# Optimization experiments

Measured on AMD Instinct MI355X. Metric: run time of the kernel, lower is better.

## Reference

```python
import jax, jax.numpy as jnp
import numpy as np

N_ATOMS = 131072
N_EDGES = 524288
N_MOLS = 2048
D = 128      # n_atom_basis
F = 128      # n_filters
G = 50       # n_gaussians
T = 3        # interaction blocks
CUTOFF = 5.0
LOG2 = float(np.log(2.0))


def ssp(x):
    # shifted softplus: ln(0.5*e^x + 0.5) = softplus(x) - ln 2
    return jax.nn.softplus(x) - LOG2


def setup_inputs() -> dict:
    key = jax.random.key(0)
    ks = jax.random.split(key, 20)
    s = 0.05
    z = jax.random.randint(ks[0], (N_ATOMS,), 1, 100, dtype=jnp.int32)
    xyz = jax.random.normal(ks[1], (N_ATOMS, 3), dtype=jnp.float32) * 3.0
    a0 = jax.random.randint(ks[2], (N_EDGES,), 0, N_ATOMS, dtype=jnp.int32)
    off = jax.random.randint(ks[3], (N_EDGES,), 1, N_ATOMS, dtype=jnp.int32)
    a = jnp.stack([a0, (a0 + off) % N_ATOMS], axis=1)  # distinct endpoints
    mol_id = jnp.sort(jax.random.randint(ks[4], (N_ATOMS,), 0, N_MOLS, dtype=jnp.int32))
    emb = (jax.random.normal(ks[5], (100, D)) * s).at[0].set(0.0)  # padding_idx=0
    return dict(
        xyz=xyz,
        emb=emb,
        fw1=jax.random.normal(ks[6], (T, G, F)) * s,
        fb1=jnp.zeros((T, F)),
        fw2=jax.random.normal(ks[7], (T, F, F)) * s,
        fb2=jnp.zeros((T, F)),
        win=jax.random.normal(ks[8], (T, D, F)) * s,
        wout1=jax.random.normal(ks[9], (T, F, D)) * s,
        bout1=jnp.zeros((T, D)),
        wout2=jax.random.normal(ks[10], (T, D, D)) * s,
        bout2=jnp.zeros((T, D)),
        wa1=jax.random.normal(ks[11], (D, D // 2)) * s,
        ba1=jnp.zeros((D // 2,)),
        wa2=jax.random.normal(ks[12], (D // 2, 1)) * s,
        ba2=jnp.zeros((1,)),
        z=z, a=a, mol_id=mol_id,
    )


def reference(xyz, emb, fw1, fb1, fw2, fb2, win, wout1, bout1, wout2, bout2,
              wa1, ba1, wa2, ba2, z, a, mol_id):
    r = emb[z]                                            # [N, D] atom embeddings
    # edge distances: e = ||xyz[a0] - xyz[a1]||  -> [E, 1]
    d = jnp.sqrt(((xyz[a[:, 0]] - xyz[a[:, 1]]) ** 2).sum(-1))[:, None]
    # Gaussian smearing on [0, cutoff]
    offsets = jnp.linspace(0.0, CUTOFF, G)
    width = offsets[1] - offsets[0]
    g = jnp.exp((-0.5 / width ** 2) * (d - offsets) ** 2)  # [E, G]
    # smooth cosine cutoff (cutoff_soft)
    C = 0.5 * (jnp.cos(d * jnp.pi / CUTOFF) + 1.0)          # [E, 1]
    for t in range(T):
        # continuous filter network on edge features
        W = ssp(g @ fw1[t] + fb1[t]) @ fw2[t] + fb2[t]      # [E, F]
        W = W * C
        h = r @ win[t]                                      # in2f, no bias [N, F]
        # symmetric gather-filter-scatter over undirected edge list
        y = jnp.zeros_like(h)
        y = y.at[a[:, 0]].add(h[a[:, 1]] * W)
        y = y.at[a[:, 1]].add(h[a[:, 0]] * W)
        dr = ssp(y @ wout1[t] + bout1[t]) @ wout2[t] + bout2[t]
        r = r + dr                                          # residual update
    # atomwise energy head
    r = ssp(r @ wa1 + ba1) @ wa2 + ba2                      # [N, 1]
    # per-molecule sum pooling (torch.split + sum)
    return jax.ops.segment_sum(r, mol_id, num_segments=N_MOLS)  # [N_MOLS, 1]
```

## Files before the change

kernel.cpp:

```cpp
#include <hip/hip_runtime.h>
#include <hip/hip_bf16.h>

#define N_ATOMS 131072
#define N_EDGES 524288
#define N_MOLS  2048
#define DD      128
#define FF      128
#define GG      50
#define TT      3

typedef __hip_bfloat16 bf16;
typedef __attribute__((ext_vector_type(8))) short short8;
typedef __attribute__((ext_vector_type(4))) float floatx4;

__device__ __forceinline__ float b2f(bf16 v) { return __bfloat162float(v); }
__device__ __forceinline__ bf16  f2b(float v) { return __float2bfloat16(v); }

__device__ __forceinline__ unsigned short f2bu(float f) {
    unsigned u = __float_as_uint(f);
    u += 0x7fff + ((u >> 16) & 1);
    return (unsigned short)(u >> 16);
}
__device__ __forceinline__ bf16 f2b_fast(float f) {
    union { unsigned short u; bf16 b; } c; c.u = f2bu(f); return c.b;
}
__device__ __forceinline__ unsigned int pk2(float lo, float hi) {
    return ((unsigned)f2bu(hi) << 16) | f2bu(lo);
}

__device__ __forceinline__ float2 up2(unsigned int u) {
    float2 f;
    f.x = __uint_as_float(u << 16);
    f.y = __uint_as_float(u & 0xffff0000u);
    return f;
}

__device__ __forceinline__ float sspf(float x) {
    float e = __expf(-fabsf(x));
    return fmaxf(x, 0.f) + __logf(1.f + e) - 0.69314718056f;
}

__device__ __forceinline__ void fma8(float* ac, uint4 wv, uint4 hv) {
    float2 w0 = up2(wv.x), h0 = up2(hv.x);
    float2 w1 = up2(wv.y), h1 = up2(hv.y);
    float2 w2 = up2(wv.z), h2 = up2(hv.z);
    float2 w3 = up2(wv.w), h3 = up2(hv.w);
    ac[0] = fmaf(w0.x, h0.x, ac[0]); ac[1] = fmaf(w0.y, h0.y, ac[1]);
    ac[2] = fmaf(w1.x, h1.x, ac[2]); ac[3] = fmaf(w1.y, h1.y, ac[3]);
    ac[4] = fmaf(w2.x, h2.x, ac[4]); ac[5] = fmaf(w2.y, h2.y, ac[5]);
    ac[6] = fmaf(w3.x, h3.x, ac[6]); ac[7] = fmaf(w3.y, h3.y, ac[7]);
}

template <int NCT>
__device__ __forceinline__ void mfma_half(const bf16* A, const bf16* B,
                                          floatx4 (&acc)[2][NCT],
                                          int kA, int wave, int q, int ln) {
#pragma unroll
    for (int k0 = 0; k0 < 64; k0 += 32) {
        short8 a0 = *(const short8*)(A + (wave * 32 + ln) * 136 + kA + k0 + q * 8);
        short8 a1 = *(const short8*)(A + (wave * 32 + 16 + ln) * 136 + kA + k0 + q * 8);
#pragma unroll
        for (int ct = 0; ct < NCT; ct++) {
            short8 b = *(const short8*)(B + (ct * 16 + ln) * 72 + k0 + q * 8);
            acc[0][ct] = __builtin_amdgcn_mfma_f32_16x16x32_bf16(a0, b, acc[0][ct], 0, 0, 0);
            acc[1][ct] = __builtin_amdgcn_mfma_f32_16x16x32_bf16(a1, b, acc[1][ct], 0, 0, 0);
        }
    }
}

template <int NCT>
__device__ __forceinline__ void mfma64(const bf16* A, const bf16* B,
                                       floatx4 (&acc)[NCT],
                                       int kA, int wave, int q, int ln) {
#pragma unroll
    for (int k0 = 0; k0 < 64; k0 += 32) {
        short8 a = *(const short8*)(A + (wave * 16 + ln) * 136 + kA + k0 + q * 8);
#pragma unroll
        for (int ct = 0; ct < NCT; ct++) {
            short8 b = *(const short8*)(B + (ct * 16 + ln) * 72 + k0 + q * 8);
            acc[ct] = __builtin_amdgcn_mfma_f32_16x16x32_bf16(a, b, acc[ct], 0, 0, 0);
        }
    }
}

__device__ __forceinline__ void stage_b(bf16* B, const bf16* WT, int k0,
                                        int nrows, int ldk, int tid) {
    for (int i = tid; i < nrows * 8; i += 256) {
        int n = i >> 3, kc = i & 7;
        *(short8*)(B + n * 72 + kc * 8) =
            *(const short8*)(WT + n * ldk + k0 + kc * 8);
    }
}

__global__ __launch_bounds__(256) void k_init(const float* __restrict__ emb,
                                              const int* __restrict__ z,
                                              bf16* __restrict__ rb) {
    int idx = blockIdx.x * 256 + threadIdx.x;
    int atom = idx >> 4, seg = idx & 15;
    const float* src = emb + (size_t)z[atom] * DD + seg * 8;
    float4 v0 = *(const float4*)(src);
    float4 v1 = *(const float4*)(src + 4);
    uint4 o;
    o.x = pk2(v0.x, v0.y); o.y = pk2(v0.z, v0.w);
    o.z = pk2(v1.x, v1.y); o.w = pk2(v1.z, v1.w);
    *(uint4*)(rb + (size_t)atom * DD + seg * 8) = o;
}

__global__ __launch_bounds__(256) void k_dist(const float* __restrict__ xyz,
                                              const int* __restrict__ a,
                                              float* __restrict__ dArr,
                                              float* __restrict__ cArr,
                                              float* __restrict__ molE) {
    int e = blockIdx.x * 256 + threadIdx.x;
    if (e < N_MOLS) molE[e] = 0.f;
    int A0 = a[2 * e], A1 = a[2 * e + 1];
    float dx = xyz[3 * A0]     - xyz[3 * A1];
    float dy = xyz[3 * A0 + 1] - xyz[3 * A1 + 1];
    float dz = xyz[3 * A0 + 2] - xyz[3 * A1 + 2];
    float d = sqrtf(dx * dx + dy * dy + dz * dz);
    dArr[e] = d;
    cArr[e] = 0.5f * (__cosf(d * 0.6283185307179586f) + 1.f);
}

__global__ __launch_bounds__(256) void k_wt(const float* __restrict__ fw1,
                                            const float* __restrict__ fw2,
                                            const float* __restrict__ win,
                                            const float* __restrict__ wout1,
                                            const float* __restrict__ wout2,
                                            const float* __restrict__ wa1,
                                            bf16* __restrict__ fw1T, bf16* __restrict__ fw2T,
                                            bf16* __restrict__ winT, bf16* __restrict__ wout1T,
                                            bf16* __restrict__ wout2T, bf16* __restrict__ wa1T) {
    int idx = blockIdx.x * 256 + threadIdx.x;
    if (idx < 3 * 128 * 64) {
        int t = idx / 8192, j = idx % 8192;
        int n = j >> 6, k = j & 63;
        fw1T[idx] = (k < GG) ? f2b(fw1[t * GG * FF + k * FF + n]) : f2b(0.f);
        return;
    }
    idx -= 3 * 128 * 64;
    if (idx < 3 * 16384) { int t = idx / 16384, j = idx % 16384; int n = j >> 7, k = j & 127;
        fw2T[idx] = f2b(fw2[t * 16384 + k * 128 + n]); return; }
    idx -= 3 * 16384;
    if (idx < 3 * 16384) { int t = idx / 16384, j = idx % 16384; int n = j >> 7, k = j & 127;
        winT[idx] = f2b(win[t * 16384 + k * 128 + n]); return; }
    idx -= 3 * 16384;
    if (idx < 3 * 16384) { int t = idx / 16384, j = idx % 16384; int n = j >> 7, k = j & 127;
        wout1T[idx] = f2b(wout1[t * 16384 + k * 128 + n]); return; }
    idx -= 3 * 16384;
    if (idx < 3 * 16384) { int t = idx / 16384, j = idx % 16384; int n = j >> 7, k = j & 127;
        wout2T[idx] = f2b(wout2[t * 16384 + k * 128 + n]); return; }
    idx -= 3 * 16384;
    if (idx < 64 * 128) { int n = idx >> 7, k = idx & 127;
        wa1T[idx] = f2b(wa1[k * 64 + n]); return; }
}

__global__ __launch_bounds__(256) void k_zero(int* __restrict__ p, int n) {
    int i = blockIdx.x * 256 + threadIdx.x;
    if (i < n) p[i] = 0;
}

__global__ __launch_bounds__(256) void k_count2(const int* __restrict__ a,
                                                int* __restrict__ cntA,
                                                int* __restrict__ cnt1,
                                                float* __restrict__ molE) {
    int e = blockIdx.x * 256 + threadIdx.x;
    if (e < N_MOLS) molE[e] = 0.f;
    atomicAdd(&cntA[a[2 * e]], 1);
    atomicAdd(&cnt1[a[2 * e + 1]], 1);
}

__global__ __launch_bounds__(256) void k_scan1(const int* __restrict__ counts,
                                               int* __restrict__ bsum) {
    __shared__ int red[256];
    int tid = threadIdx.x;
    int i0 = blockIdx.x * 512 + tid * 2;
    red[tid] = counts[i0] + counts[i0 + 1];
    __syncthreads();
    for (int off = 128; off > 0; off >>= 1) {
        if (tid < off) red[tid] += red[tid + off];
        __syncthreads();
    }
    if (tid == 0) bsum[blockIdx.x] = red[0];
}

__global__ __launch_bounds__(256) void k_scan2(int* __restrict__ bsum,
                                               int* __restrict__ ptr) {
    __shared__ int v[256];
    int tid = threadIdx.x;
    v[tid] = bsum[tid];
    __syncthreads();
    if (tid == 0) {
        int acc = 0;
        for (int i = 0; i < 256; i++) { int t = v[i]; v[i] = acc; acc += t; }
        ptr[N_ATOMS] = acc;
    }
    __syncthreads();
    bsum[tid] = v[tid];
}

__global__ __launch_bounds__(256) void k_scan3(int* __restrict__ counts,
                                               const int* __restrict__ bsum,
                                               int* __restrict__ ptr) {
    __shared__ int red[256];
    int tid = threadIdx.x;
    int i0 = blockIdx.x * 512 + tid * 2;
    int c0 = counts[i0], c1 = counts[i0 + 1];
    int s = c0 + c1;
    red[tid] = s;
    __syncthreads();
    for (int off = 1; off < 256; off <<= 1) {
        int t = (tid >= off) ? red[tid - off] : 0;
        __syncthreads();
        red[tid] += t;
        __syncthreads();
    }
    int base = bsum[blockIdx.x] + red[tid] - s;
    ptr[i0] = base;
    ptr[i0 + 1] = base + c0;
    counts[i0] = base;
    counts[i0 + 1] = base + c0;
}

__global__ __launch_bounds__(256) void k_permA(const float* __restrict__ xyz,
                                               const int* __restrict__ a,
                                               int* __restrict__ cursorA,
                                               int* __restrict__ cursor1,
                                               float* __restrict__ dAp,
                                               float* __restrict__ cAp,
                                               int* __restrict__ a1s,
                                               int* __restrict__ adj1) {
    int e = blockIdx.x * 256 + threadIdx.x;
    int A0 = a[2 * e], A1 = a[2 * e + 1];
    float dx = xyz[3 * A0]     - xyz[3 * A1];
    float dy = xyz[3 * A0 + 1] - xyz[3 * A1 + 1];
    float dz = xyz[3 * A0 + 2] - xyz[3 * A1 + 2];
    float d = sqrtf(dx * dx + dy * dy + dz * dz);
    int newe = atomicAdd(&cursorA[A0], 1);
    dAp[newe] = d;
    cAp[newe] = 0.5f * (__cosf(d * 0.6283185307179586f) + 1.f);
    a1s[newe] = A1;
    int slot = atomicAdd(&cursor1[A1], 1);
    adj1[2 * slot] = newe;
    adj1[2 * slot + 1] = A0;
}

struct SmemHE {
    bf16 A[64][136];
    bf16 B[128][72];
    float dS[64], cS[64], b1S[128], b2S[128];
};

__device__ __forceinline__ void h_part(SmemHE& sm, int blk,
                                       const bf16* __restrict__ rb,
                                       const bf16* __restrict__ winT_t,
                                       bf16* __restrict__ h) {
    int tid = threadIdx.x, n0 = blk * 64;
    for (int i = tid; i < 64 * 16; i += 256) {
        int row = i >> 4, seg = i & 15;
        *(uint4*)(&sm.A[row][seg * 8]) =
            *(const uint4*)(rb + (size_t)(n0 + row) * DD + seg * 8);
    }
    stage_b(&sm.B[0][0], winT_t, 0, 128, 128, tid);
    __syncthreads();
    int wave = tid >> 6, lane = tid & 63, q = lane >> 4, ln = lane & 15;
    floatx4 acc[8];
#pragma unroll
    for (int j = 0; j < 8; j++) acc[j] = (floatx4){0.f, 0.f, 0.f, 0.f};
    mfma64<8>(&sm.A[0][0], &sm.B[0][0], acc, 0, wave, q, ln);
    __syncthreads();
    stage_b(&sm.B[0][0], winT_t, 64, 128, 128, tid);
    __syncthreads();
    mfma64<8>(&sm.A[0][0], &sm.B[0][0], acc, 64, wave, q, ln);
#pragma unroll
    for (int ct = 0; ct < 8; ct++)
#pragma unroll
        for (int rg = 0; rg < 4; rg++) {
            int row = wave * 16 + q * 4 + rg, col = ct * 16 + ln;
            sm.A[row][col] = f2b_fast(acc[ct][rg]);
        }
    __syncthreads();
    for (int i = tid; i < 64 * 16; i += 256) {
        int row = i >> 4, seg = i & 15;
        *(uint4*)(h + (size_t)(n0 + row) * FF + seg * 8) =
            *(const uint4*)(&sm.A[row][seg * 8]);
    }
}

__device__ __forceinline__ void edge_part(SmemHE& sm, int blk,
                                          const float* __restrict__ dAp,
                                          const float* __restrict__ cAp,
                                          const bf16* __restrict__ fw1T_t,
                                          const float* __restrict__ fb1_t,
                                          const bf16* __restrict__ fw2T_t,
                                          const float* __restrict__ fb2_t,
                                          bf16* __restrict__ Wt) {
    int tid = threadIdx.x, e0 = blk * 64;
    if (tid < 64) { sm.dS[tid] = dAp[e0 + tid]; sm.cS[tid] = cAp[e0 + tid]; }
    if (tid < 128) { sm.b1S[tid] = fb1_t[tid]; sm.b2S[tid] = fb2_t[tid]; }
    stage_b(&sm.B[0][0], fw1T_t, 0, 128, 64, tid);
    __syncthreads();
    const float width = 5.0f / 49.0f;
    const float coeff = -0.5f / (width * width);
    for (int idx = tid; idx < 64 * 32; idx += 256) {
        int i = idx >> 5, kp = (idx & 31) * 2;
        float d = sm.dS[i];
        float t0 = d - (float)kp * width;
        float t1 = d - (float)(kp + 1) * width;
        float v0 = (kp < GG)     ? __expf(coeff * t0 * t0) : 0.f;
        float v1 = (kp + 1 < GG) ? __expf(coeff * t1 * t1) : 0.f;
        *(unsigned int*)(&sm.A[i][kp]) = pk2(v0, v1);
    }
    __syncthreads();
    int wave = tid >> 6, lane = tid & 63, q = lane >> 4, ln = lane & 15;
    floatx4 acc[8];
#pragma unroll
    for (int j = 0; j < 8; j++) acc[j] = (floatx4){0.f, 0.f, 0.f, 0.f};
    mfma64<8>(&sm.A[0][0], &sm.B[0][0], acc, 0, wave, q, ln);
#pragma unroll
    for (int ct = 0; ct < 8; ct++)
#pragma unroll
        for (int rg = 0; rg < 4; rg++) {
            int row = wave * 16 + q * 4 + rg, col = ct * 16 + ln;
            sm.A[row][col] = f2b_fast(sspf(acc[ct][rg] + sm.b1S[col]));
        }
    __syncthreads();
    stage_b(&sm.B[0][0], fw2T_t, 0, 128, 128, tid);
    __syncthreads();
#pragma unroll
    for (int j = 0; j < 8; j++) acc[j] = (floatx4){0.f, 0.f, 0.f, 0.f};
    mfma64<8>(&sm.A[0][0], &sm.B[0][0], acc, 0, wave, q, ln);
    __syncthreads();
    stage_b(&sm.B[0][0], fw2T_t, 64, 128, 128, tid);
    __syncthreads();
    mfma64<8>(&sm.A[0][0], &sm.B[0][0], acc, 64, wave, q, ln);
#pragma unroll
    for (int ct = 0; ct < 8; ct++)
#pragma unroll
        for (int rg = 0; rg < 4; rg++) {
            int row = wave * 16 + q * 4 + rg, col = ct * 16 + ln;
            sm.A[row][col] = f2b_fast((acc[ct][rg] + sm.b2S[col]) * sm.cS[row]);
        }
    __syncthreads();
    for (int i = tid; i < 64 * 16; i += 256) {
        int row = i >> 4, seg = i & 15;
        *(uint4*)(Wt + (size_t)(e0 + row) * FF + seg * 8) =
            *(const uint4*)(&sm.A[row][seg * 8]);
    }
}

__global__ __launch_bounds__(256, 4) void k_he(const bf16* __restrict__ rb,
                                               const bf16* __restrict__ winT_t,
                                               bf16* __restrict__ h,
                                               const float* __restrict__ dAp,
                                               const float* __restrict__ cAp,
                                               const bf16* __restrict__ fw1T_t,
                                               const float* __restrict__ fb1_t,
                                               const bf16* __restrict__ fw2T_t,
                                               const float* __restrict__ fb2_t,
                                               bf16* __restrict__ Wt) {
    __shared__ SmemHE sm;
    int bi = blockIdx.x;
    if (bi % 5 == 0)
        h_part(sm, bi / 5, rb, winT_t, h);
    else
        edge_part(sm, bi - bi / 5 - 1, dAp, cAp, fw1T_t, fb1_t, fw2T_t, fb2_t, Wt);
}

__global__ __launch_bounds__(256, 5) void k_gather_node64(const int* __restrict__ baseA,
                                                          const int* __restrict__ a1s,
                                                          const int* __restrict__ ptr1,
                                                          const int* __restrict__ adj1,
                                                          const bf16* __restrict__ Wt,
                                                          const bf16* __restrict__ h,
                                                          const bf16* __restrict__ wout1T_t,
                                                          const float* __restrict__ bo1_t,
                                                          const bf16* __restrict__ wout2T_t,
                                                          const float* __restrict__ bo2_t,
                                                          bf16* __restrict__ rb) {
    __shared__ __align__(16) bf16 A[64][136];
    __shared__ __align__(16) bf16 B[64][72];
    __shared__ float b1S[128], b2S[128];
    int tid = threadIdx.x, n0 = blockIdx.x * 64;
    if (tid < 128) { b1S[tid] = bo1_t[tid]; b2S[tid] = bo2_t[tid]; }
    stage_b(&B[0][0], wout1T_t, 0, 64, 128, tid);
    int wave = tid >> 6, lane = tid & 63;
    int seg = lane & 15;
    int rg  = lane >> 4;
    for (int k = 0; k < 16; k += 2) {
        int rowA = wave * 16 + k;
        int atomA = n0 + rowA;
        int2 b01 = *(const int2*)(baseA + atomA);
        int b2v = baseA[atomA + 2];
        int2 p01 = *(const int2*)(ptr1 + atomA);
        int p2v = ptr1[atomA + 2];
        int sA0 = b01.x + rg, eA0v = b01.y;
        int sB0 = b01.y + rg, eB0v = b2v;
        int sA1 = p01.x + rg, eA1v = p01.y;
        int sB1 = p01.y + rg, eB1v = p2v;
        int oA = (sA0 < eA0v) ? a1s[sA0] : 0;
        int oB = (sB0 < eB0v) ? a1s[sB0] : 0;
        int2 eoA = (sA1 < eA1v) ? *(const int2*)(adj1 + 2 * sA1) : make_int2(0, 0);
        int2 eoB = (sB1 < eB1v) ? *(const int2*)(adj1 + 2 * sB1) : make_int2(0, 0);
        float acA[8], acB[8];
#pragma unroll
        for (int j = 0; j < 8; j++) { acA[j] = 0.f; acB[j] = 0.f; }
        while ((sA0 < eA0v) | (sA1 < eA1v) | (sB0 < eB0v) | (sB1 < eB1v)) {
            bool pA0 = sA0 < eA0v, pA1 = sA1 < eA1v;
            bool pB0 = sB0 < eB0v, pB1 = sB1 < eB1v;
            uint4 wvA0, hvA0, wvA1, hvA1, wvB0, hvB0, wvB1, hvB1;
            if (pA0) {
                wvA0 = *(const uint4*)(Wt + (size_t)sA0 * FF + seg * 8);
                hvA0 = *(const uint4*)(h + (size_t)oA * FF + seg * 8);
            }
            if (pA1) {
                wvA1 = *(const uint4*)(Wt + (size_t)eoA.x * FF + seg * 8);
                hvA1 = *(const uint4*)(h + (size_t)eoA.y * FF + seg * 8);
            }
            if (pB0) {
                wvB0 = *(const uint4*)(Wt + (size_t)sB0 * FF + seg * 8);
                hvB0 = *(const uint4*)(h + (size_t)oB * FF + seg * 8);
            }
            if (pB1) {
                wvB1 = *(const uint4*)(Wt + (size_t)eoB.x * FF + seg * 8);
                hvB1 = *(const uint4*)(h + (size_t)eoB.y * FF + seg * 8);
            }
            int sA0n = sA0 + 4, sA1n = sA1 + 4, sB0n = sB0 + 4, sB1n = sB1 + 4;
            int oAn = (sA0n < eA0v) ? a1s[sA0n] : 0;
            int oBn = (sB0n < eB0v) ? a1s[sB0n] : 0;
            int2 eoAn = (sA1n < eA1v) ? *(const int2*)(adj1 + 2 * sA1n) : make_int2(0, 0);
            int2 eoBn = (sB1n < eB1v) ? *(const int2*)(adj1 + 2 * sB1n) : make_int2(0, 0);
            if (pA0) fma8(acA, wvA0, hvA0);
            if (pA1) fma8(acA, wvA1, hvA1);
            if (pB0) fma8(acB, wvB0, hvB0);
            if (pB1) fma8(acB, wvB1, hvB1);
            sA0 = sA0n; sA1 = sA1n; sB0 = sB0n; sB1 = sB1n;
            oA = oAn; oB = oBn; eoA = eoAn; eoB = eoBn;
        }
#pragma unroll
        for (int j = 0; j < 8; j++) {
            float vA = acA[j], vB = acB[j];
            vA += __shfl_down(vA, 32); vB += __shfl_down(vB, 32);
            vA += __shfl_down(vA, 16); vB += __shfl_down(vB, 16);
            acA[j] = vA; acB[j] = vB;
        }
        if (rg == 0) {
            uint4 oU;
            oU.x = pk2(acA[0], acA[1]); oU.y = pk2(acA[2], acA[3]);
            oU.z = pk2(acA[4], acA[5]); oU.w = pk2(acA[6], acA[7]);
            *(uint4*)(&A[rowA][seg * 8]) = oU;
            oU.x = pk2(acB[0], acB[1]); oU.y = pk2(acB[2], acB[3]);
            oU.z = pk2(acB[4], acB[5]); oU.w = pk2(acB[6], acB[7]);
            *(uint4*)(&A[rowA + 1][seg * 8]) = oU;
        }
    }
    __syncthreads();
    int q = lane >> 4, ln = lane & 15;
    floatx4 acc[8];
#pragma unroll
    for (int j = 0; j < 8; j++) acc[j] = (floatx4){0.f, 0.f, 0.f, 0.f};
    mfma64<4>(&A[0][0], &B[0][0], *(floatx4(*)[4])(&acc[0]), 0, wave, q, ln);
    __syncthreads();
    stage_b(&B[0][0], wout1T_t + 64 * 128, 0, 64, 128, tid);
    __syncthreads();
    mfma64<4>(&A[0][0], &B[0][0], *(floatx4(*)[4])(&acc[4]), 0, wave, q, ln);
    __syncthreads();
    stage_b(&B[0][0], wout1T_t, 64, 64, 128, tid);
    __syncthreads();
    mfma64<4>(&A[0][0], &B[0][0], *(floatx4(*)[4])(&acc[0]), 64, wave, q, ln);
    __syncthreads();
    stage_b(&B[0][0], wout1T_t + 64 * 128, 64, 64, 128, tid);
    __syncthreads();
    mfma64<4>(&A[0][0], &B[0][0], *(floatx4(*)[4])(&acc[4]), 64, wave, q, ln);
#pragma unroll
    for (int cc = 0; cc < 8; cc++)
#pragma unroll
        for (int rgi = 0; rgi < 4; rgi++) {
            int row = wave * 16 + q * 4 + rgi;
            int col = (cc >> 2) * 64 + (cc & 3) * 16 + ln;
            A[row][col] = f2b_fast(sspf(acc[cc][rgi] + b1S[col]));
        }
    __syncthreads();
    stage_b(&B[0][0], wout2T_t, 0, 64, 128, tid);
    __syncthreads();
#pragma unroll
    for (int j = 0; j < 8; j++) acc[j] = (floatx4){0.f, 0.f, 0.f, 0.f};
    mfma64<4>(&A[0][0], &B[0][0], *(floatx4(*)[4])(&acc[0]), 0, wave, q, ln);
    __syncthreads();
    stage_b(&B[0][0], wout2T_t + 64 * 128, 0, 64, 128, tid);
    __syncthreads();
    mfma64<4>(&A[0][0], &B[0][0], *(floatx4(*)[4])(&acc[4]), 0, wave, q, ln);
    __syncthreads();
    stage_b(&B[0][0], wout2T_t, 64, 64, 128, tid);
    __syncthreads();
    mfma64<4>(&A[0][0], &B[0][0], *(floatx4(*)[4])(&acc[0]), 64, wave, q, ln);
    __syncthreads();
    stage_b(&B[0][0], wout2T_t + 64 * 128, 64, 64, 128, tid);
    __syncthreads();
    mfma64<4>(&A[0][0], &B[0][0], *(floatx4(*)[4])(&acc[4]), 64, wave, q, ln);
#pragma unroll
    for (int cc = 0; cc < 8; cc++)
#pragma unroll
        for (int rgi = 0; rgi < 4; rgi++) {
            int row = wave * 16 + q * 4 + rgi;
            int col = (cc >> 2) * 64 + (cc & 3) * 16 + ln;
            size_t off = (size_t)(n0 + row) * DD + col;
            rb[off] = f2b_fast(b2f(rb[off]) + acc[cc][rgi] + b2S[col]);
        }
}

__global__ __launch_bounds__(256) void k_h(const bf16* __restrict__ rb,
                                           const bf16* __restrict__ winT_t,
                                           bf16* __restrict__ h,
                                           float* __restrict__ y) {
    __shared__ __align__(16) bf16 A[128][136];
    __shared__ __align__(16) bf16 B[128][72];
    int tid = threadIdx.x, n0 = blockIdx.x * 128;
    for (int i = tid; i < 128 * 16; i += 256) {
        int row = i >> 4, seg = i & 15;
        *(uint4*)(&A[row][seg * 8]) =
            *(const uint4*)(rb + (size_t)(n0 + row) * DD + seg * 8);
        *(float4*)(y + (size_t)(n0 + row) * FF + seg * 8) = (float4){0.f, 0.f, 0.f, 0.f};
        *(float4*)(y + (size_t)(n0 + row) * FF + seg * 8 + 4) = (float4){0.f, 0.f, 0.f, 0.f};
    }
    stage_b(&B[0][0], winT_t, 0, 128, 128, tid);
    __syncthreads();
    int wave = tid >> 6, lane = tid & 63, q = lane >> 4, ln = lane & 15;
    floatx4 acc[2][8];
#pragma unroll
    for (int i = 0; i < 2; i++)
#pragma unroll
        for (int j = 0; j < 8; j++) acc[i][j] = (floatx4){0.f, 0.f, 0.f, 0.f};
    mfma_half<8>(&A[0][0], &B[0][0], acc, 0, wave, q, ln);
    __syncthreads();
    stage_b(&B[0][0], winT_t, 64, 128, 128, tid);
    __syncthreads();
    mfma_half<8>(&A[0][0], &B[0][0], acc, 64, wave, q, ln);
#pragma unroll
    for (int rt = 0; rt < 2; rt++)
#pragma unroll
        for (int ct = 0; ct < 8; ct++)
#pragma unroll
            for (int rg = 0; rg < 4; rg++) {
                int row = wave * 32 + rt * 16 + q * 4 + rg, col = ct * 16 + ln;
                h[(size_t)(n0 + row) * FF + col] = f2b(acc[rt][ct][rg]);
            }
}

__global__ __launch_bounds__(256) void k_edge(const float* __restrict__ dArr,
                                              const float* __restrict__ cArr,
                                              const int* __restrict__ a,
                                              const bf16* __restrict__ fw1T_t,
                                              const float* __restrict__ fb1_t,
                                              const bf16* __restrict__ fw2T_t,
                                              const float* __restrict__ fb2_t,
                                              const bf16* __restrict__ h,
                                              float* __restrict__ y) {
    __shared__ __align__(16) bf16 A[128][136];
    __shared__ __align__(16) bf16 B[128][72];
    __shared__ float dS[128], cS[128], b1S[128], b2S[128];
    __shared__ int a0S[128], a1S[128];
    int tid = threadIdx.x, e0 = blockIdx.x * 128;
    if (tid < 128) {
        int e = e0 + tid;
        dS[tid] = dArr[e]; cS[tid] = cArr[e];
        a0S[tid] = a[2 * e]; a1S[tid] = a[2 * e + 1];
        b1S[tid] = fb1_t[tid]; b2S[tid] = fb2_t[tid];
    }
    stage_b(&B[0][0], fw1T_t, 0, 128, 64, tid);
    __syncthreads();
    const float width = 5.0f / 49.0f;
    const float coeff = -0.5f / (width * width);
    for (int idx = tid; idx < 128 * 64; idx += 256) {
        int i = idx >> 6, k = idx & 63;
        float v = 0.f;
        if (k < GG) { float t = dS[i] - (float)k * width; v = __expf(coeff * t * t); }
        A[i][k] = f2b(v);
// ... 55 lines not shown
    int tid = threadIdx.x, n0 = blockIdx.x * 128;
    if (tid < 128) { b1S[tid] = bo1_t[tid]; b2S[tid] = bo2_t[tid]; }
    for (int idx = tid; idx < 128 * 128; idx += 256) {
        int row = idx >> 7, col = idx & 127;
        A[row][col] = f2b(y[(size_t)(n0 + row) * FF + col]);
    }
    stage_b(&B[0][0], wout1T_t, 0, 128, 128, tid);
    __syncthreads();
    int wave = tid >> 6, lane = tid & 63, q = lane >> 4, ln = lane & 15;
    floatx4 acc[2][8];
#pragma unroll
    for (int i = 0; i < 2; i++)
#pragma unroll
        for (int j = 0; j < 8; j++) acc[i][j] = (floatx4){0.f, 0.f, 0.f, 0.f};
    mfma_half<8>(&A[0][0], &B[0][0], acc, 0, wave, q, ln);
    __syncthreads();
    stage_b(&B[0][0], wout1T_t, 64, 128, 128, tid);
    __syncthreads();
    mfma_half<8>(&A[0][0], &B[0][0], acc, 64, wave, q, ln);
#pragma unroll
    for (int rt = 0; rt < 2; rt++)
#pragma unroll
        for (int ct = 0; ct < 8; ct++)
#pragma unroll
            for (int rg = 0; rg < 4; rg++) {
                int row = wave * 32 + rt * 16 + q * 4 + rg, col = ct * 16 + ln;
                A[row][col] = f2b(sspf(acc[rt][ct][rg] + b1S[col]));
            }
    __syncthreads();
    stage_b(&B[0][0], wout2T_t, 0, 128, 128, tid);
    __syncthreads();
#pragma unroll
    for (int i = 0; i < 2; i++)
#pragma unroll
        for (int j = 0; j < 8; j++) acc[i][j] = (floatx4){0.f, 0.f, 0.f, 0.f};
    mfma_half<8>(&A[0][0], &B[0][0], acc, 0, wave, q, ln);
    __syncthreads();
    stage_b(&B[0][0], wout2T_t, 64, 128, 128, tid);
    __syncthreads();
    mfma_half<8>(&A[0][0], &B[0][0], acc, 64, wave, q, ln);
#pragma unroll
    for (int rt = 0; rt < 2; rt++)
#pragma unroll
        for (int ct = 0; ct < 8; ct++)
#pragma unroll
            for (int rg = 0; rg < 4; rg++) {
                int row = wave * 32 + rt * 16 + q * 4 + rg, col = ct * 16 + ln;
                size_t off = (size_t)(n0 + row) * DD + col;
                rb[off] = f2b_fast(b2f(rb[off]) + acc[rt][ct][rg] + b2S[col]);
            }
}

__global__ __launch_bounds__(256) void k_head(const bf16* __restrict__ rb,
                                              const bf16* __restrict__ wa1T,
                                              const float* __restrict__ ba1,
                                              const float* __restrict__ wa2,
                                              const float* __restrict__ ba2,
                                              const int* __restrict__ mol,
                                              float* __restrict__ molE) {
    __shared__ __align__(16) bf16 A[128][136];
    __shared__ __align__(16) bf16 B[64][72];
    __shared__ __align__(16) bf16 U[128][72];
    __shared__ float wa2S[64], ba1S[64];
    int tid = threadIdx.x, n0 = blockIdx.x * 128;
    if (tid < 64) { wa2S[tid] = wa2[tid]; ba1S[tid] = ba1[tid]; }
    for (int i = tid; i < 128 * 16; i += 256) {
        int row = i >> 4, seg = i & 15;
        *(uint4*)(&A[row][seg * 8]) =
            *(const uint4*)(rb + (size_t)(n0 + row) * DD + seg * 8);
    }
    stage_b(&B[0][0], wa1T, 0, 64, 128, tid);
    __syncthreads();
    int wave = tid >> 6, lane = tid & 63, q = lane >> 4, ln = lane & 15;
    floatx4 acc[2][4];
#pragma unroll
    for (int i = 0; i < 2; i++)
#pragma unroll
        for (int j = 0; j < 4; j++) acc[i][j] = (floatx4){0.f, 0.f, 0.f, 0.f};
    mfma_half<4>(&A[0][0], &B[0][0], acc, 0, wave, q, ln);
    __syncthreads();
    stage_b(&B[0][0], wa1T, 64, 64, 128, tid);
    __syncthreads();
    mfma_half<4>(&A[0][0], &B[0][0], acc, 64, wave, q, ln);
#pragma unroll
    for (int rt = 0; rt < 2; rt++)
#pragma unroll
        for (int ct = 0; ct < 4; ct++)
#pragma unroll
            for (int rg = 0; rg < 4; rg++) {
                int row = wave * 32 + rt * 16 + q * 4 + rg, col = ct * 16 + ln;
                U[row][col] = f2b_fast(acc[rt][ct][rg] + ba1S[col]);
            }
    __syncthreads();
    if (tid < 128) {
        float s = ba2[0];
#pragma unroll
        for (int j = 0; j < 64; j++) s += sspf(b2f(U[tid][j])) * wa2S[j];
        atomicAdd(&molE[mol[n0 + tid]], s);
    }
}

__global__ __launch_bounds__(256) void k_out(const float* __restrict__ molE,
                                             float* __restrict__ out) {
    int i = blockIdx.x * 256 + threadIdx.x;
    out[i] = molE[i];
}

extern "C" void kernel_launch(void* const* d_in, const int* in_sizes, int n_in,
                              void* d_out, int out_size, void* d_ws, size_t ws_size,
                              hipStream_t stream) {
    const float* xyz   = (const float*)d_in[0];
    const float* emb   = (const float*)d_in[1];
    const float* fw1   = (const float*)d_in[2];
    const float* fb1   = (const float*)d_in[3];
    const float* fw2   = (const float*)d_in[4];
    const float* fb2   = (const float*)d_in[5];
    const float* win   = (const float*)d_in[6];
    const float* wout1 = (const float*)d_in[7];
    const float* bout1 = (const float*)d_in[8];
    const float* wout2 = (const float*)d_in[9];
    const float* bout2 = (const float*)d_in[10];
    const float* wa1   = (const float*)d_in[11];
    const float* ba1   = (const float*)d_in[12];
    const float* wa2   = (const float*)d_in[13];
    const float* ba2   = (const float*)d_in[14];
    const int*  z     = (const int*)d_in[15];
    const int*  a     = (const int*)d_in[16];
    const int*  mol   = (const int*)d_in[17];

    char* ws = (char*)d_ws;
    bf16*  rb   = (bf16*) ws; ws += (size_t)N_ATOMS * DD * 2;
    bf16*  h    = (bf16*) ws; ws += (size_t)N_ATOMS * FF * 2;
    float* molE = (float*)ws; ws += (size_t)N_MOLS * 4;
    float* dAp  = (float*)ws; ws += (size_t)N_EDGES * 4;
    float* cAp  = (float*)ws; ws += (size_t)N_EDGES * 4;
    bf16*  fw1T   = (bf16*)ws; ws += 3 * 128 * 64 * 2;
    bf16*  fw2T   = (bf16*)ws; ws += 3 * 128 * 128 * 2;
    bf16*  winT   = (bf16*)ws; ws += 3 * 128 * 128 * 2;
    bf16*  wout1T = (bf16*)ws; ws += 3 * 128 * 128 * 2;
    bf16*  wout2T = (bf16*)ws; ws += 3 * 128 * 128 * 2;
    bf16*  wa1T   = (bf16*)ws; ws += 64 * 128 * 2;
    char*  csr_base = ws;
    int*   baseA   = (int*)ws; ws += 524320;
    int*   ptr1    = (int*)ws; ws += 524320;
    int*   cursorA = (int*)ws; ws += (size_t)N_ATOMS * 4;
    int*   cursor1 = (int*)ws; ws += (size_t)N_ATOMS * 4;
    int*   a1s     = (int*)ws; ws += (size_t)N_EDGES * 4;
    int*   adj1    = (int*)ws; ws += (size_t)2 * N_EDGES * 4;
    int*   bsumA   = (int*)ws; ws += 1024;
    int*   bsum1   = (int*)ws; ws += 1024;
    bf16*  Wt      = (bf16*)ws; ws += (size_t)N_EDGES * FF * 2;
    size_t need = (size_t)(ws - (char*)d_ws);

    k_init<<<N_ATOMS * 16 / 256, 256, 0, stream>>>(emb, z, rb);
    k_wt<<<896, 256, 0, stream>>>(fw1, fw2, win, wout1, wout2, wa1,
                                  fw1T, fw2T, winT, wout1T, wout2T, wa1T);

    if (ws_size >= need) {
        k_zero<<<(N_ATOMS + 255) / 256, 256, 0, stream>>>(cursorA, N_ATOMS);
        k_zero<<<(N_ATOMS + 255) / 256, 256, 0, stream>>>(cursor1, N_ATOMS);
        k_count2<<<N_EDGES / 256, 256, 0, stream>>>(a, cursorA, cursor1, molE);
        k_scan1<<<256, 256, 0, stream>>>(cursorA, bsumA);
        k_scan2<<<1, 256, 0, stream>>>(bsumA, baseA);
        k_scan3<<<256, 256, 0, stream>>>(cursorA, bsumA, baseA);
        k_scan1<<<256, 256, 0, stream>>>(cursor1, bsum1);
        k_scan2<<<1, 256, 0, stream>>>(bsum1, ptr1);
        k_scan3<<<256, 256, 0, stream>>>(cursor1, bsum1, ptr1);
        k_permA<<<N_EDGES / 256, 256, 0, stream>>>(xyz, a, cursorA, cursor1,
                                                   dAp, cAp, a1s, adj1);
        for (int t = 0; t < TT; t++) {
            k_he<<<N_ATOMS / 64 + N_EDGES / 64, 256, 0, stream>>>(
                rb, winT + t * 16384, h, dAp, cAp,
                fw1T + t * 8192, fb1 + t * FF,
                fw2T + t * 16384, fb2 + t * FF, Wt);
            k_gather_node64<<<N_ATOMS / 64, 256, 0, stream>>>(
                baseA, a1s, ptr1, adj1, Wt, h,
                wout1T + t * 16384, bout1 + t * DD,
                wout2T + t * 16384, bout2 + t * DD, rb);
        }
    } else {
        float* y = (float*)csr_base;
        k_dist<<<N_EDGES / 256, 256, 0, stream>>>(xyz, a, dAp, cAp, molE);
        for (int t = 0; t < TT; t++) {
            k_h<<<N_ATOMS / 128, 256, 0, stream>>>(rb, winT + t * 16384, h, y);
            k_edge<<<N_EDGES / 128, 256, 0, stream>>>(dAp, cAp, a,
                                                      fw1T + t * 8192, fb1 + t * FF,
                                                      fw2T + t * 16384, fb2 + t * FF, h, y);
            k_node<<<N_ATOMS / 128, 256, 0, stream>>>(y, wout1T + t * 16384, bout1 + t * DD,
                                                      wout2T + t * 16384, bout2 + t * DD, rb);
        }
    }
    k_head<<<N_ATOMS / 128, 256, 0, stream>>>(rb, wa1T, ba1, wa2, ba2, mol, molE);
    k_out<<<N_MOLS / 256, 256, 0, stream>>>(molE, (float*)d_out);
}
```

Before: 993.9 us.

## Enlarge h/edge MFMA tiles to 128 rows, merge setup kernels, nontemporal Wt loads

The fused h/edge kernel now processes 128 rows per block, with each wave computing two 16-row tiles against a 64-column B slice staged in four passes. This halves the block count and amortizes weight staging over more rows, at the cost of more LDS and registers (occupancy hint lowered from 4 to 3). The setup kernels are merged: init and weight transpose become one launch, the two zero kernels become one, and the paired scans are joined, which cuts launch overhead. Wt loads in the gather kernel now use nontemporal hints so the streamed filter values do not evict the reused h rows from cache.

```diff
diff --git a/kernel.cpp b/kernel.cpp
--- a/kernel.cpp
+++ b/kernel.cpp
@@ -12,6 +12,7 @@
 typedef __hip_bfloat16 bf16;
 typedef __attribute__((ext_vector_type(8))) short short8;
 typedef __attribute__((ext_vector_type(4))) float floatx4;
+typedef unsigned int uint4e __attribute__((ext_vector_type(4)));
 
 __device__ __forceinline__ float b2f(bf16 v) { return __bfloat162float(v); }
 __device__ __forceinline__ bf16  f2b(float v) { return __float2bfloat16(v); }
@@ -33,6 +34,11 @@
     f.x = __uint_as_float(u << 16);
     f.y = __uint_as_float(u & 0xffff0000u);
     return f;
+}
+
+__device__ __forceinline__ uint4 ntload(const bf16* p) {
+    uint4e v = __builtin_nontemporal_load((const uint4e*)p);
+    union { uint4e e; uint4 u; } c; c.e = v; return c.u;
 }
 
 __device__ __forceinline__ float sspf(float x) {
@@ -69,6 +75,23 @@
 }
 
 template <int NCT>
+__device__ __forceinline__ void mfma_halfo(const bf16* A, const bf16* B,
+                                           floatx4 (&acc)[2][8], int ctBase,
+                                           int kA, int wave, int q, int ln) {
+#pragma unroll
+    for (int k0 = 0; k0 < 64; k0 += 32) {
+        short8 a0 = *(const short8*)(A + (wave * 32 + ln) * 136 + kA + k0 + q * 8);
+        short8 a1 = *(const short8*)(A + (wave * 32 + 16 + ln) * 136 + kA + k0 + q * 8);
+#pragma unroll
+        for (int ct = 0; ct < NCT; ct++) {
+            short8 b = *(const short8*)(B + (ct * 16 + ln) * 72 + k0 + q * 8);
+            acc[0][ctBase + ct] = __builtin_amdgcn_mfma_f32_16x16x32_bf16(a0, b, acc[0][ctBase + ct], 0, 0, 0);
+            acc[1][ctBase + ct] = __builtin_amdgcn_mfma_f32_16x16x32_bf16(a1, b, acc[1][ctBase + ct], 0, 0, 0);
+        }
+    }
+}
+
+template <int NCT>
 __device__ __forceinline__ void mfma64(const bf16* A, const bf16* B,
                                        floatx4 (&acc)[NCT],
                                        int kA, int wave, int q, int ln) {
@@ -92,46 +115,32 @@
     }
 }
 
-__global__ __launch_bounds__(256) void k_init(const float* __restrict__ emb,
-                                              const int* __restrict__ z,
-                                              bf16* __restrict__ rb) {
-    int idx = blockIdx.x * 256 + threadIdx.x;
-    int atom = idx >> 4, seg = idx & 15;
-    const float* src = emb + (size_t)z[atom] * DD + seg * 8;
-    float4 v0 = *(const float4*)(src);
-    float4 v1 = *(const float4*)(src + 4);
-    uint4 o;
-    o.x = pk2(v0.x, v0.y); o.y = pk2(v0.z, v0.w);
-    o.z = pk2(v1.x, v1.y); o.w = pk2(v1.z, v1.w);
-    *(uint4*)(rb + (size_t)atom * DD + seg * 8) = o;
-}
-
-__global__ __launch_bounds__(256) void k_dist(const float* __restrict__ xyz,
-                                              const int* __restrict__ a,
-                                              float* __restrict__ dArr,
-                                              float* __restrict__ cArr,
-                                              float* __restrict__ molE) {
-    int e = blockIdx.x * 256 + threadIdx.x;
-    if (e < N_MOLS) molE[e] = 0.f;
-    int A0 = a[2 * e], A1 = a[2 * e + 1];
-    float dx = xyz[3 * A0]     - xyz[3 * A1];
-    float dy = xyz[3 * A0 + 1] - xyz[3 * A1 + 1];
-    float dz = xyz[3 * A0 + 2] - xyz[3 * A1 + 2];
-    float d = sqrtf(dx * dx + dy * dy + dz * dz);
-    dArr[e] = d;
-    cArr[e] = 0.5f * (__cosf(d * 0.6283185307179586f) + 1.f);
-}
-
-__global__ __launch_bounds__(256) void k_wt(const float* __restrict__ fw1,
-                                            const float* __restrict__ fw2,
-                                            const float* __restrict__ win,
-                                            const float* __restrict__ wout1,
-                                            const float* __restrict__ wout2,
-                                            const float* __restrict__ wa1,
-                                            bf16* __restrict__ fw1T, bf16* __restrict__ fw2T,
-                                            bf16* __restrict__ winT, bf16* __restrict__ wout1T,
-                                            bf16* __restrict__ wout2T, bf16* __restrict__ wa1T) {
-    int idx = blockIdx.x * 256 + threadIdx.x;
+__global__ __launch_bounds__(256) void k_initwt(const float* __restrict__ emb,
+                                                const int* __restrict__ z,
+                                                bf16* __restrict__ rb,
+                                                const float* __restrict__ fw1,
+                                                const float* __restrict__ fw2,
+                                                const float* __restrict__ win,
+                                                const float* __restrict__ wout1,
+                                                const float* __restrict__ wout2,
+                                                const float* __restrict__ wa1,
+                                                bf16* __restrict__ fw1T, bf16* __restrict__ fw2T,
+                                                bf16* __restrict__ winT, bf16* __restrict__ wout1T,
+                                                bf16* __restrict__ wout2T, bf16* __restrict__ wa1T) {
+    int bi = blockIdx.x;
+    if (bi < N_ATOMS * 16 / 256) {
+        int idx = bi * 256 + threadIdx.x;
+        int atom = idx >> 4, seg = idx & 15;
+        const float* src = emb + (size_t)z[atom] * DD + seg * 8;
+        float4 v0 = *(const float4*)(src);
+        float4 v1 = *(const float4*)(src + 4);
+        uint4 o;
+        o.x = pk2(v0.x, v0.y); o.y = pk2(v0.z, v0.w);
+        o.z = pk2(v1.x, v1.y); o.w = pk2(v1.z, v1.w);
+        *(uint4*)(rb + (size_t)atom * DD + seg * 8) = o;
+        return;
+    }
+    int idx = (bi - N_ATOMS * 16 / 256) * 256 + threadIdx.x;
     if (idx < 3 * 128 * 64) {
         int t = idx / 8192, j = idx % 8192;
         int n = j >> 6, k = j & 63;
@@ -155,9 +164,27 @@
         wa1T[idx] = f2b(wa1[k * 64 + n]); return; }
 }
 
-__global__ __launch_bounds__(256) void k_zero(int* __restrict__ p, int n) {
+__global__ __launch_bounds__(256) void k_dist(const float* __restrict__ xyz,
+                                              const int* __restrict__ a,
+                                              float* __restrict__ dArr,
+                                              float* __restrict__ cArr,
+                                              float* __restrict__ molE) {
+    int e = blockIdx.x * 256 + threadIdx.x;
+    if (e < N_MOLS) molE[e] = 0.f;
+    int A0 = a[2 * e], A1 = a[2 * e + 1];
+    float dx = xyz[3 * A0]     - xyz[3 * A1];
+    float dy = xyz[3 * A0 + 1] - xyz[3 * A1 + 1];
+    float dz = xyz[3 * A0 + 2] - xyz[3 * A1 + 2];
+    float d = sqrtf(dx * dx + dy * dy + dz * dz);
+    dArr[e] = d;
+    cArr[e] = 0.5f * (__cosf(d * 0.6283185307179586f) + 1.f);
+}
+
+__global__ __launch_bounds__(256) void k_zero2(int* __restrict__ pA,
+                                               int* __restrict__ p1) {
     int i = blockIdx.x * 256 + threadIdx.x;
-    if (i < n) p[i] = 0;
+    if (i < N_ATOMS) pA[i] = 0;
+    else p1[i - N_ATOMS] = 0;
 }
 
 __global__ __launch_bounds__(256) void k_count2(const int* __restrict__ a,
@@ -170,41 +197,60 @@
     atomicAdd(&cnt1[a[2 * e + 1]], 1);
 }
 
-__global__ __launch_bounds__(256) void k_scan1(const int* __restrict__ counts,
-                                               int* __restrict__ bsum) {
+__global__ __launch_bounds__(256) void k_scan1j(const int* __restrict__ cursorA,
+                                                const int* __restrict__ cursor1,
+                                                int* __restrict__ bsumA,
+                                                int* __restrict__ bsum1) {
     __shared__ int red[256];
     int tid = threadIdx.x;
-    int i0 = blockIdx.x * 512 + tid * 2;
+    int arr = blockIdx.x >> 8, b = blockIdx.x & 255;
+    const int* counts = arr ? cursor1 : cursorA;
+    int* bsum = arr ? bsum1 : bsumA;
+    int i0 = b * 512 + tid * 2;
     red[tid] = counts[i0] + counts[i0 + 1];
     __syncthreads();
     for (int off = 128; off > 0; off >>= 1) {
         if (tid < off) red[tid] += red[tid + off];
         __syncthreads();
     }
-    if (tid == 0) bsum[blockIdx.x] = red[0];
-}
-
-__global__ __launch_bounds__(256) void k_scan2(int* __restrict__ bsum,
-                                               int* __restrict__ ptr) {
+    if (tid == 0) bsum[b] = red[0];
+}
+
+__global__ __launch_bounds__(256) void k_scan2j(int* __restrict__ bsumA,
+                                                int* __restrict__ bsum1,
+                                                int* __restrict__ baseA,
+                                                int* __restrict__ ptr1) {
     __shared__ int v[256];
     int tid = threadIdx.x;
-    v[tid] = bsum[tid];
-    __syncthreads();
-    if (tid == 0) {
-        int acc = 0;
-        for (int i = 0; i < 256; i++) { int t = v[i]; v[i] = acc; acc += t; }
-        ptr[N_ATOMS] = acc;
-    }
-    __syncthreads();
-    bsum[tid] = v[tid];
-}
-
-__global__ __launch_bounds__(256) void k_scan3(int* __restrict__ counts,
-                                               const int* __restrict__ bsum,
-                                               int* __restrict__ ptr) {
+    for (int arr = 0; arr < 2; arr++) {
+        int* bsum = arr ? bsum1 : bsumA;
+        int* ptrN = arr ? ptr1 : baseA;
+        v[tid] = bsum[tid];
+        __syncthreads();
+        if (tid == 0) {
+            int acc = 0;
+            for (int i = 0; i < 256; i++) { int t = v[i]; v[i] = acc; acc += t; }
+            ptrN[N_ATOMS] = acc;
+        }
+        __syncthreads();
+        bsum[tid] = v[tid];
+        __syncthreads();
+    }
+}
+
+__global__ __launch_bounds__(256) void k_scan3j(int* __restrict__ cursorA,
+                                                int* __restrict__ cursor1,
+                                                const int* __restrict__ bsumA,
+                                                const int* __restrict__ bsum1,
+                                                int* __restrict__ baseA,
+                                                int* __restrict__ ptr1) {
     __shared__ int red[256];
     int tid = threadIdx.x;
-    int i0 = blockIdx.x * 512 + tid * 2;
+    int arr = blockIdx.x >> 8, b = blockIdx.x & 255;
+    int* counts = arr ? cursor1 : cursorA;
+    const int* bsum = arr ? bsum1 : bsumA;
+    int* ptr = arr ? ptr1 : baseA;
+    int i0 = b * 512 + tid * 2;
     int c0 = counts[i0], c1 = counts[i0 + 1];
     int s = c0 + c1;
     red[tid] = s;
@@ -215,7 +261,7 @@
         red[tid] += t;
         __syncthreads();
     }
-    int base = bsum[blockIdx.x] + red[tid] - s;
+    int base = bsum[b] + red[tid] - s;
     ptr[i0] = base;
     ptr[i0 + 1] = base + c0;
     counts[i0] = base;
@@ -246,63 +292,80 @@
 }
 
 struct SmemHE {
-    bf16 A[64][136];
-    bf16 B[128][72];
-    float dS[64], cS[64], b1S[128], b2S[128];
+    bf16 A[128][136];
+    bf16 B[64][72];
+    float dS[128], cS[128], b1S[128], b2S[128];
 };
 
-__device__ __forceinline__ void h_part(SmemHE& sm, int blk,
-                                       const bf16* __restrict__ rb,
-                                       const bf16* __restrict__ winT_t,
-                                       bf16* __restrict__ h) {
-    int tid = threadIdx.x, n0 = blk * 64;
-    for (int i = tid; i < 64 * 16; i += 256) {
+__device__ __forceinline__ void h_part128(SmemHE& sm, int blk,
+                                          const bf16* __restrict__ rb,
+                                          const bf16* __restrict__ winT_t,
+                                          bf16* __restrict__ h) {
+    int tid = threadIdx.x, n0 = blk * 128;
+    for (int i = tid; i < 128 * 16; i += 256) {
         int row = i >> 4, seg = i & 15;
         *(uint4*)(&sm.A[row][seg * 8]) =
             *(const uint4*)(rb + (size_t)(n0 + row) * DD + seg * 8);
     }
-    stage_b(&sm.B[0][0], winT_t, 0, 128, 128, tid);
+    stage_b(&sm.B[0][0], winT_t, 0, 64, 128, tid);
     __syncthreads();
     int wave = tid >> 6, lane = tid & 63, q = lane >> 4, ln = lane & 15;
-    floatx4 acc[8];
-#pragma unroll
-    for (int j = 0; j < 8; j++) acc[j] = (floatx4){0.f, 0.f, 0.f, 0.f};
-    mfma64<8>(&sm.A[0][0], &sm.B[0][0], acc, 0, wave, q, ln);
-    __syncthreads();
-    stage_b(&sm.B[0][0], winT_t, 64, 128, 128, tid);
-    __syncthreads();
-    mfma64<8>(&sm.A[0][0], &sm.B[0][0], acc, 64, wave, q, ln);
-#pragma unroll
-    for (int ct = 0; ct < 8; ct++)
-#pragma unroll
-        for (int rg = 0; rg < 4; rg++) {
-            int row = wave * 16 + q * 4 + rg, col = ct * 16 + ln;
-            sm.A[row][col] = f2b_fast(acc[ct][rg]);
-        }
-    __syncthreads();
-    for (int i = tid; i < 64 * 16; i += 256) {
+    floatx4 acc[2][8];
+#pragma unroll
+    for (int i = 0; i < 2; i++)
+#pragma unroll
+        for (int j = 0; j < 8; j++) acc[i][j] = (floatx4){0.f, 0.f, 0.f, 0.f};
+    mfma_halfo<4>(&sm.A[0][0], &sm.B[0][0], acc, 0, 0, wave, q, ln);
+    __syncthreads();
+    stage_b(&sm.B[0][0], winT_t + 64 * 128, 0, 64, 128, tid);
+    __syncthreads();
+    mfma_halfo<4>(&sm.A[0][0], &sm.B[0][0], acc, 4, 0, wave, q, ln);
+    __syncthreads();
+    stage_b(&sm.B[0][0], winT_t, 64, 64, 128, tid);
+    __syncthreads();
+    mfma_halfo<4>(&sm.A[0][0], &sm.B[0][0], acc, 0, 64, wave, q, ln);
+    __syncthreads();
+    stage_b(&sm.B[0][0], winT_t + 64 * 128, 64, 64, 128, tid);
+    __syncthreads();
+    mfma_halfo<4>(&sm.A[0][0], &sm.B[0][0], acc, 4, 64, wave, q, ln);
+#pragma unroll
+    for (int rt = 0; rt < 2; rt++)
+#pragma unroll
+        for (int cc = 0; cc < 8; cc++)
+#pragma unroll
+            for (int rg = 0; rg < 4; rg++) {
+                int row = wave * 32 + rt * 16 + q * 4 + rg;
+                int col = (cc >> 2) * 64 + (cc & 3) * 16 + ln;
+                sm.A[row][col] = f2b_fast(acc[rt][cc][rg]);
+            }
+    __syncthreads();
+    for (int i = tid; i < 128 * 16; i += 256) {
         int row = i >> 4, seg = i & 15;
         *(uint4*)(h + (size_t)(n0 + row) * FF + seg * 8) =
             *(const uint4*)(&sm.A[row][seg * 8]);
     }
 }
 
-__device__ __forceinline__ void edge_part(SmemHE& sm, int blk,
-                                          const float* __restrict__ dAp,
-                                          const float* __restrict__ cAp,
-                                          const bf16* __restrict__ fw1T_t,
-                                          const float* __restrict__ fb1_t,
-                                          const bf16* __restrict__ fw2T_t,
-                                          const float* __restrict__ fb2_t,
-                                          bf16* __restrict__ Wt) {
-    int tid = threadIdx.x, e0 = blk * 64;
-    if (tid < 64) { sm.dS[tid] = dAp[e0 + tid]; sm.cS[tid] = cAp[e0 + tid]; }
-    if (tid < 128) { sm.b1S[tid] = fb1_t[tid]; sm.b2S[tid] = fb2_t[tid]; }
-    stage_b(&sm.B[0][0], fw1T_t, 0, 128, 64, tid);
+__device__ __forceinline__ void edge_part128(SmemHE& sm, int blk,
+                                             const float* __restrict__ dAp,
+                                             const float* __restrict__ cAp,
+                                             const bf16* __restrict__ fw1T_t,
+                                             const float* __restrict__ fb1_t,
+                                             const bf16* __restrict__ fw2T_t,
+                                             const float* __restrict__ fb2_t,
+                                             bf16* __restrict__ Wt) {
+    int tid = threadIdx.x, e0 = blk * 128;
+    if (tid < 128) {
+        sm.dS[tid] = dAp[e0 + tid];
+        sm.cS[tid] = cAp[e0 + tid];
+        sm.b1S[tid] = fb1_t[tid];
+        sm.b2S[tid] = fb2_t[tid];
+    }
+    stage_b(&sm.B[0][0], fw1T_t, 0, 64, 64, tid);
     __syncthreads();
     const float width = 5.0f / 49.0f;
     const float coeff = -0.5f / (width * width);
-    for (int idx = tid; idx < 64 * 32; idx += 256) {
+    for (int idx = tid; idx < 128 * 32; idx += 256) {
         int i = idx >> 5, kp = (idx & 31) * 2;
         float d = sm.dS[i];
         float t0 = d - (float)kp * width;
@@ -313,43 +376,65 @@
     }
     __syncthreads();
     int wave = tid >> 6, lane = tid & 63, q = lane >> 4, ln = lane & 15;
-    floatx4 acc[8];
-#pragma unroll
-    for (int j = 0; j < 8; j++) acc[j] = (floatx4){0.f, 0.f, 0.f, 0.f};
-    mfma64<8>(&sm.A[0][0], &sm.B[0][0], acc, 0, wave, q, ln);
-#pragma unroll
-    for (int ct = 0; ct < 8; ct++)
-#pragma unroll
-        for (int rg = 0; rg < 4; rg++) {
-            int row = wave * 16 + q * 4 + rg, col = ct * 16 + ln;
-            sm.A[row][col] = f2b_fast(sspf(acc[ct][rg] + sm.b1S[col]));
-        }
-    __syncthreads();
-    stage_b(&sm.B[0][0], fw2T_t, 0, 128, 128, tid);
-    __syncthreads();
-#pragma unroll
-    for (int j = 0; j < 8; j++) acc[j] = (floatx4){0.f, 0.f, 0.f, 0.f};
-    mfma64<8>(&sm.A[0][0], &sm.B[0][0], acc, 0, wave, q, ln);
-    __syncthreads();
-    stage_b(&sm.B[0][0], fw2T_t, 64, 128, 128, tid);
-    __syncthreads();
-    mfma64<8>(&sm.A[0][0], &sm.B[0][0], acc, 64, wave, q, ln);
-#pragma unroll
-    for (int ct = 0; ct < 8; ct++)
-#pragma unroll
-        for (int rg = 0; rg < 4; rg++) {
-            int row = wave * 16 + q * 4 + rg, col = ct * 16 + ln;
-            sm.A[row][col] = f2b_fast((acc[ct][rg] + sm.b2S[col]) * sm.cS[row]);
-        }
-    __syncthreads();
-    for (int i = tid; i < 64 * 16; i += 256) {
+    floatx4 acc[2][8];
+#pragma unroll
+    for (int i = 0; i < 2; i++)
+#pragma unroll
+        for (int j = 0; j < 8; j++) acc[i][j] = (floatx4){0.f, 0.f, 0.f, 0.f};
+    mfma_halfo<4>(&sm.A[0][0], &sm.B[0][0], acc, 0, 0, wave, q, ln);
+    __syncthreads();
+    stage_b(&sm.B[0][0], fw1T_t + 64 * 64, 0, 64, 64, tid);
+    __syncthreads();
+    mfma_halfo<4>(&sm.A[0][0], &sm.B[0][0], acc, 4, 0, wave, q, ln);
+#pragma unroll
+    for (int rt = 0; rt < 2; rt++)
+#pragma unroll
+        for (int cc = 0; cc < 8; cc++)
+#pragma unroll
+            for (int rg = 0; rg < 4; rg++) {
+                int row = wave * 32 + rt * 16 + q * 4 + rg;
+                int col = (cc >> 2) * 64 + (cc & 3) * 16 + ln;
+                sm.A[row][col] = f2b_fast(sspf(acc[rt][cc][rg] + sm.b1S[col]));
+            }
+    __syncthreads();
+    stage_b(&sm.B[0][0], fw2T_t, 0, 64, 128, tid);
+    __syncthreads();
+#pragma unroll
+    for (int i = 0; i < 2; i++)
+#pragma unroll
+        for (int j = 0; j < 8; j++) acc[i][j] = (floatx4){0.f, 0.f, 0.f, 0.f};
+    mfma_halfo<4>(&sm.A[0][0], &sm.B[0][0], acc, 0, 0, wave, q, ln);
+    __syncthreads();
+    stage_b(&sm.B[0][0], fw2T_t + 64 * 128, 0, 64, 128, tid);
+    __syncthreads();
+    mfma_halfo<4>(&sm.A[0][0], &sm.B[0][0], acc, 4, 0, wave, q, ln);
+    __syncthreads();
+    stage_b(&sm.B[0][0], fw2T_t, 64, 64, 128, tid);
+    __syncthreads();
+    mfma_halfo<4>(&sm.A[0][0], &sm.B[0][0], acc, 0, 64, wave, q, ln);
+    __syncthreads();
+    stage_b(&sm.B[0][0], fw2T_t + 64 * 128, 64, 64, 128, tid);
+    __syncthreads();
+    mfma_halfo<4>(&sm.A[0][0], &sm.B[0][0], acc, 4, 64, wave, q, ln);
+#pragma unroll
+    for (int rt = 0; rt < 2; rt++)
+#pragma unroll
+        for (int cc = 0; cc < 8; cc++)
+#pragma unroll
+            for (int rg = 0; rg < 4; rg++) {
+                int row = wave * 32 + rt * 16 + q * 4 + rg;
+                int col = (cc >> 2) * 64 + (cc & 3) * 16 + ln;
+                sm.A[row][col] = f2b_fast((acc[rt][cc][rg] + sm.b2S[col]) * sm.cS[row]);
+            }
+    __syncthreads();
+    for (int i = tid; i < 128 * 16; i += 256) {
         int row = i >> 4, seg = i & 15;
         *(uint4*)(Wt + (size_t)(e0 + row) * FF + seg * 8) =
             *(const uint4*)(&sm.A[row][seg * 8]);
     }
 }
 
-__global__ __launch_bounds__(256, 4) void k_he(const bf16* __restrict__ rb,
+__global__ __launch_bounds__(256, 3) void k_he(const bf16* __restrict__ rb,
                                                const bf16* __restrict__ winT_t,
                                                bf16* __restrict__ h,
                                                const float* __restrict__ dAp,
@@ -362,9 +447,9 @@
     __shared__ SmemHE sm;
     int bi = blockIdx.x;
     if (bi % 5 == 0)
-        h_part(sm, bi / 5, rb, winT_t, h);
+        h_part128(sm, bi / 5, rb, winT_t, h);
     else
-        edge_part(sm, bi - bi / 5 - 1, dAp, cAp, fw1T_t, fb1_t, fw2T_t, fb2_t, Wt);
+        edge_part128(sm, bi - bi / 5 - 1, dAp, cAp, fw1T_t, fb1_t, fw2T_t, fb2_t, Wt);
 }
 
 __global__ __launch_bounds__(256, 5) void k_gather_node64(const int* __restrict__ baseA,
@@ -410,19 +495,19 @@
             bool pB0 = sB0 < eB0v, pB1 = sB1 < eB1v;
             uint4 wvA0, hvA0, wvA1, hvA1, wvB0, hvB0, wvB1, hvB1;
             if (pA0) {
-                wvA0 = *(const uint4*)(Wt + (size_t)sA0 * FF + seg * 8);
+                wvA0 = ntload(Wt + (size_t)sA0 * FF + seg * 8);
                 hvA0 = *(const uint4*)(h + (size_t)oA * FF + seg * 8);
             }
             if (pA1) {
-                wvA1 = *(const uint4*)(Wt + (size_t)eoA.x * FF + seg * 8);
+                wvA1 = ntload(Wt + (size_t)eoA.x * FF + seg * 8);
                 hvA1 = *(const uint4*)(h + (size_t)eoA.y * FF + seg * 8);
             }
             if (pB0) {
-                wvB0 = *(const uint4*)(Wt + (size_t)sB0 * FF + seg * 8);
+                wvB0 = ntload(Wt + (size_t)sB0 * FF + seg * 8);
                 hvB0 = *(const uint4*)(h + (size_t)oB * FF + seg * 8);
             }
             if (pB1) {
-                wvB1 = *(const uint4*)(Wt + (size_t)eoB.x * FF + seg * 8);
+                wvB1 = ntload(Wt + (size_t)eoB.x * FF + seg * 8);
                 hvB1 = *(const uint4*)(h + (size_t)eoB.y * FF + seg * 8);
             }
             int sA0n = sA0 + 4, sA1n = sA1 + 4, sB0n = sB0 + 4, sB1n = sB1 + 4;
@@ -784,24 +869,20 @@
     bf16*  Wt      = (bf16*)ws; ws += (size_t)N_EDGES * FF * 2;
     size_t need = (size_t)(ws - (char*)d_ws);
 
-    k_init<<<N_ATOMS * 16 / 256, 256, 0, stream>>>(emb, z, rb);
-    k_wt<<<896, 256, 0, stream>>>(fw1, fw2, win, wout1, wout2, wa1,
-                                  fw1T, fw2T, winT, wout1T, wout2T, wa1T);
+    k_initwt<<<N_ATOMS * 16 / 256 + 896, 256, 0, stream>>>(
+        emb, z, rb, fw1, fw2, win, wout1, wout2, wa1,
+        fw1T, fw2T, winT, wout1T, wout2T, wa1T);
 
     if (ws_size >= need) {
-        k_zero<<<(N_ATOMS + 255) / 256, 256, 0, stream>>>(cursorA, N_ATOMS);
-        k_zero<<<(N_ATOMS + 255) / 256, 256, 0, stream>>>(cursor1, N_ATOMS);
+        k_zero2<<<2 * N_ATOMS / 256, 256, 0, stream>>>(cursorA, cursor1);
         k_count2<<<N_EDGES / 256, 256, 0, stream>>>(a, cursorA, cursor1, molE);
-        k_scan1<<<256, 256, 0, stream>>>(cursorA, bsumA);
-        k_scan2<<<1, 256, 0, stream>>>(bsumA, baseA);
-        k_scan3<<<256, 256, 0, stream>>>(cursorA, bsumA, baseA);
-        k_scan1<<<256, 256, 0, stream>>>(cursor1, bsum1);
-        k_scan2<<<1, 256, 0, stream>>>(bsum1, ptr1);
-        k_scan3<<<256, 256, 0, stream>>>(cursor1, bsum1, ptr1);
+        k_scan1j<<<512, 256, 0, stream>>>(cursorA, cursor1, bsumA, bsum1);
+        k_scan2j<<<1, 256, 0, stream>>>(bsumA, bsum1, baseA, ptr1);
+        k_scan3j<<<512, 256, 0, stream>>>(cursorA, cursor1, bsumA, bsum1, baseA, ptr1);
         k_permA<<<N_EDGES / 256, 256, 0, stream>>>(xyz, a, cursorA, cursor1,
                                                    dAp, cAp, a1s, adj1);
         for (int t = 0; t < TT; t++) {
-            k_he<<<N_ATOMS / 64 + N_EDGES / 64, 256, 0, stream>>>(
+            k_he<<<N_ATOMS / 128 + N_EDGES / 128, 256, 0, stream>>>(
                 rb, winT + t * 16384, h, dAp, cAp,
                 fw1T + t * 8192, fb1 + t * FF,
                 fw2T + t * 16384, fb2 + t * FF, Wt);
```

Result: slower. 1.062 ms (+6.8%).
